# Optimization experiments

Measured on AMD Instinct MI355X. Metric: run time of the kernel, lower is better.

## Reference

```python
import jax, jax.numpy as jnp
import numpy as np
import math

B, L, HID = 2, 1024, 1536
NH, HD = 24, 64
DSSM = NH * HD            # 1536 (expand = 1)
QKV = 3 * DSSM
DCONV = 2
EPS = 1e-6


def _silu(u):
    return u * jax.nn.sigmoid(u)


def setup_inputs() -> dict:
    key = jax.random.key(0)
    ks = jax.random.split(key, 10)
    x = jax.random.normal(ks[0], (B, L, HID), dtype=jnp.float32)
    w_qkv = jax.random.normal(ks[1], (QKV, HID), dtype=jnp.float32) / math.sqrt(HID)
    conv_w = jax.random.normal(ks[2], (QKV, DCONV), dtype=jnp.float32) * 0.5  # depthwise causal conv, k=2
    w_dt = jax.random.normal(ks[3], (NH, HID), dtype=jnp.float32) * 0.02
    # dt_bias init exactly as in the torch module
    dt = jnp.exp(jax.random.uniform(ks[4], (NH,)) * (math.log(0.1) - math.log(0.001)) + math.log(0.001))
    dt = jnp.clip(dt, 1e-4, None)
    dt_bias = dt + jnp.log(-jnp.expm1(-dt))
    a_log = jnp.log(jax.random.uniform(ks[5], (NH,), minval=1.0, maxval=16.0))
    D = jnp.ones((NH, HD), dtype=jnp.float32)
    w_z = jax.random.normal(ks[6], (DSSM, HID), dtype=jnp.float32) / math.sqrt(HID)
    b_z = jnp.zeros((DSSM,), dtype=jnp.float32)
    rms_w = jnp.ones((DSSM,), dtype=jnp.float32)
    w_o = jax.random.normal(ks[7], (HID, DSSM), dtype=jnp.float32) / math.sqrt(DSSM)
    return dict(x=x, w_qkv=w_qkv, conv_w=conv_w, w_dt=w_dt, dt_bias=dt_bias,
                a_log=a_log, D=D, w_z=w_z, b_z=b_z, rms_w=rms_w, w_o=w_o)


def reference(x, w_qkv, conv_w, w_dt, dt_bias, a_log, D, w_z, b_z, rms_w, w_o):
    # qkv projection  [B,L,3*DSSM]
    qkv = jnp.einsum('blh,qh->blq', x, w_qkv)
    # depthwise causal conv1d (kernel size 2, padding k-1, trimmed to L)
    prev = jnp.pad(qkv, ((0, 0), (1, 0), (0, 0)))[:, :L]
    qkv = _silu(prev * conv_w[:, 0] + qkv * conv_w[:, 1])
    q, k, v = jnp.split(qkv, 3, axis=-1)
    q = q.reshape(B, L, NH, HD)
    k = k.reshape(B, L, NH, HD)
    v = v.reshape(B, L, NH, HD)
    # dt discretization: softplus(dt_proj(x) + dt_bias)   [B,L,NH]
    dt = jax.nn.softplus(jnp.einsum('blh,nh->bln', x, w_dt) + dt_bias)
    A = -jnp.exp(a_log)              # [NH], negative
    dA = dt * A                      # [B,L,NH]
    cs = jnp.transpose(jnp.cumsum(dA, axis=1), (0, 2, 1))   # [B,NH,L]
    diff = cs[:, :, :, None] - cs[:, :, None, :]            # [B,NH,L,L], <=0 on causal part
    causal = jnp.tril(jnp.ones((L, L), dtype=bool))
    decay = jnp.exp(jnp.where(causal, diff, -jnp.inf))      # segment-sum decay matrix
    # quadratic SSD (attention) form of the selective scan
    scores = jnp.einsum('bihd,bjhd->bhij', q, k) * decay
    scores = scores * jnp.transpose(dt, (0, 2, 1))[:, :, None, :]  # dt_j on keys (B-discretization)
    y = jnp.einsum('bhij,bjhd->bihd', scores, v)
    y = y + v * D                    # D skip connection
    y = y.reshape(B, L, DSSM)
    # z gate + RMSNorm + output projection
    z = jnp.einsum('blh,dh->bld', x, w_z) + b_z
    y = y * _silu(z)
    y = y * jax.lax.rsqrt(jnp.mean(y * y, axis=-1, keepdims=True) + EPS) * rms_w
    return jnp.einsum('bld,hd->blh', y, w_o)
```

## Files before the change

kernel.cpp:

```cpp
#include <hip/hip_runtime.h>
#include <hip/hip_bf16.h>
#include <math.h>

#define B_ 2
#define L_ 1024
#define HID_ 1536
#define NH_ 24
#define HD_ 64
#define DSSM_ 1536
#define QKV_ 4608
#define M_ 2048

typedef __attribute__((ext_vector_type(8))) short short8;
typedef __attribute__((ext_vector_type(4))) short short4e;
typedef __attribute__((ext_vector_type(4))) float floatx4;

__device__ __forceinline__ void gload_lds16(const short* g, short* l)
{
    __builtin_amdgcn_global_load_lds(
        (const __attribute__((address_space(1))) void*)g,
        (__attribute__((address_space(3))) void*)l,
        16, 0, 0);
}

__device__ __forceinline__ float bfs2f(short s)
{
    unsigned u = ((unsigned)(unsigned short)s) << 16;
    float f; __builtin_memcpy(&f, &u, 4); return f;
}
__device__ __forceinline__ short f2bfs(float f)
{
    __hip_bfloat16 h = __float2bfloat16(f);
    short s; __builtin_memcpy(&s, &h, 2); return s;
}

__device__ const int kIt[30] = {0,1,2,3,4,5, 6,6, 7,7, 8,8, 9,9, 10,10, 11,11,
                                12,12,12, 13,13,13, 14,14,14, 15,15,15};
__device__ const int kS[30]  = {0,0,0,0,0,0, 0,1, 0,1, 0,1, 0,1, 0,1, 0,1,
                                0,1,2, 0,1,2, 0,1,2, 0,1,2};

#define CN0 (M_ * HID_)
#define CN1 (QKV_ * HID_)
#define CN2 (DSSM_ * HID_)
#define CN3 (HID_ * DSSM_)
__global__ void cast_all_kernel(
    const float* __restrict__ x,  const float* __restrict__ wq,
    const float* __restrict__ wz, const float* __restrict__ wo,
    __hip_bfloat16* __restrict__ xb,
    __hip_bfloat16* __restrict__ wcat,
    __hip_bfloat16* __restrict__ wob)
{
    int i = (blockIdx.x * 256 + threadIdx.x) * 4;
    const float* src; __hip_bfloat16* dst; int off;
    if (i < CN0)                   { src = x;  dst = xb;         off = i; }
    else if (i < CN0 + CN1)        { src = wq; dst = wcat;       off = i - CN0; }
    else if (i < CN0 + CN1 + CN2)  { src = wz; dst = wcat + CN1; off = i - CN0 - CN1; }
    else                           { src = wo; dst = wob;        off = i - CN0 - CN1 - CN2; }
    float4 f = *reinterpret_cast<const float4*>(src + off);
    dst[off]     = __float2bfloat16(f.x);
    dst[off + 1] = __float2bfloat16(f.y);
    dst[off + 2] = __float2bfloat16(f.z);
    dst[off + 3] = __float2bfloat16(f.w);
}

#define MFMA_ __builtin_amdgcn_mfma_f32_16x16x32_bf16
#define BAR_() __builtin_amdgcn_s_barrier()
#define DRAIN_() do { asm volatile("s_waitcnt lgkmcnt(0)" ::: "memory"); \
                      __builtin_amdgcn_sched_barrier(0); } while (0)

#define CSTR 200

__global__ __launch_bounds__(512, 1) void gemm_qkvz_256(
    const __hip_bfloat16* __restrict__ A,
    const __hip_bfloat16* __restrict__ Bm,
    __hip_bfloat16* __restrict__ qkv_out,
    float* __restrict__ z_out,
    const float* __restrict__ b_z)
{
    extern __shared__ short lds[];
    const int K  = HID_;
    const int NT = K / 64;
    const int tid   = threadIdx.x;
    const int lane  = tid & 63;
    const int wave  = tid >> 6;
    const int col16 = lane & 15;
    const int quad  = lane >> 4;
    const int wm = wave >> 2;
    const int wn = wave & 3;
    const int rowblk = blockIdx.y * 256;
    const int colblk = blockIdx.x * 192;

    const short* Ap = reinterpret_cast<const short*>(A);
    const short* Bp = reinterpret_cast<const short*>(Bm);

    const int o  = tid * 16;
    const int s  = o ^ (((o >> 7) & 7) << 4);
    const int sr = s >> 7;
    const int sc = (s & 127) >> 1;
    const int ldst = tid * 8;

    const int mask = (col16 & 7) << 4;
    const int e0 = ((quad * 16)      ^ mask) >> 1;
    const int e1 = ((64 + quad * 16) ^ mask) >> 1;
    const int arow = (wm * 128 + col16) * 64;
    const int brow = (wn * 48  + col16) * 64;

    floatx4 acc[8][3] = {};

    auto STAGE_A = [&](int c, int u, int t) {
        const short* g = Ap + (size_t)(rowblk + u * 64 + sr) * K + t * 64 + sc;
        gload_lds16(g, &lds[c * 16384 + u * 4096 + ldst]);
    };
    auto STAGE_B = [&](int c, int u, int t) {
        const short* g = Bp + (size_t)(colblk + u * 64 + sr) * K + t * 64 + sc;
        gload_lds16(g, &lds[32768 + c * 12288 + u * 4096 + ldst]);
    };

    STAGE_A(0, 0, 0); STAGE_A(0, 1, 0); STAGE_A(0, 2, 0); STAGE_A(0, 3, 0);
    STAGE_B(0, 0, 0); STAGE_B(0, 1, 0); STAGE_B(0, 2, 0);
    STAGE_A(1, 0, 1); STAGE_A(1, 1, 1); STAGE_A(1, 2, 1); STAGE_A(1, 3, 1);
    asm volatile("s_waitcnt vmcnt(4)" ::: "memory");
    __builtin_amdgcn_sched_barrier(0);
    BAR_();

    for (int t = 0; t < NT; ++t) {
        const int cur = t & 1, nxt = cur ^ 1;
        const int Ab = cur * 16384;
        const int Bb = 32768 + cur * 12288;
        short8 af0[8], af1[8], bf0[3], bf1[3];

#pragma unroll
        for (int m = 0; m < 8; ++m)
            af0[m] = *reinterpret_cast<const short8*>(&lds[Ab + arow + m * 1024 + e0]);
#pragma unroll
        for (int n = 0; n < 3; ++n)
            bf0[n] = *reinterpret_cast<const short8*>(&lds[Bb + brow + n * 1024 + e0]);
        if (t + 1 < NT) { STAGE_B(nxt, 0, t + 1); STAGE_B(nxt, 1, t + 1); }
        BAR_();
        __builtin_amdgcn_s_setprio(1);
#pragma unroll
        for (int m = 0; m < 8; ++m) {
            acc[m][0] = MFMA_(af0[m], bf0[0], acc[m][0], 0, 0, 0);
            acc[m][1] = MFMA_(af0[m], bf0[1], acc[m][1], 0, 0, 0);
        }
        __builtin_amdgcn_s_setprio(0);
        DRAIN_();
        BAR_();

#pragma unroll
        for (int m = 0; m < 8; ++m)
            af1[m] = *reinterpret_cast<const short8*>(&lds[Ab + arow + m * 1024 + e1]);
        bf1[0] = *reinterpret_cast<const short8*>(&lds[Bb + brow + e1]);
        if (t + 1 < NT) STAGE_B(nxt, 2, t + 1);
        BAR_();
        __builtin_amdgcn_s_setprio(1);
#pragma unroll
        for (int m = 0; m < 8; ++m) {
            acc[m][2] = MFMA_(af0[m], bf0[2], acc[m][2], 0, 0, 0);
            acc[m][0] = MFMA_(af1[m], bf1[0], acc[m][0], 0, 0, 0);
        }
        __builtin_amdgcn_s_setprio(0);
        DRAIN_();
        BAR_();

        bf1[1] = *reinterpret_cast<const short8*>(&lds[Bb + brow + 1024 + e1]);
        bf1[2] = *reinterpret_cast<const short8*>(&lds[Bb + brow + 2048 + e1]);
        if (t + 2 < NT) {
            STAGE_A(cur, 0, t + 2); STAGE_A(cur, 1, t + 2);
            STAGE_A(cur, 2, t + 2); STAGE_A(cur, 3, t + 2);
        }
        if (t >= NT - 2) { asm volatile("s_waitcnt vmcnt(0)" ::: "memory"); }
        else             { asm volatile("s_waitcnt vmcnt(4)" ::: "memory"); }
        __builtin_amdgcn_sched_barrier(0);
        BAR_();
        __builtin_amdgcn_s_setprio(1);
#pragma unroll
        for (int m = 0; m < 8; ++m) {
            acc[m][1] = MFMA_(af1[m], bf1[1], acc[m][1], 0, 0, 0);
            acc[m][2] = MFMA_(af1[m], bf1[2], acc[m][2], 0, 0, 0);
        }
        __builtin_amdgcn_s_setprio(0);
        DRAIN_();
        BAR_();
    }

    if (blockIdx.x < 24) {
        const int rb = wm * 128 + quad * 4;
        const int cb = wn * 48 + col16;
#pragma unroll
        for (int m = 0; m < 8; ++m)
#pragma unroll
            for (int n = 0; n < 3; ++n)
#pragma unroll
                for (int r = 0; r < 4; ++r)
                    lds[(rb + m * 16 + r) * CSTR + cb + n * 16] =
                        f2bfs(acc[m][n][r]);
        __syncthreads();
        const int row = tid >> 1;
        const int seg = tid & 1;
        const short* srcp = &lds[row * CSTR + seg * 96];
        short* dstp = reinterpret_cast<short*>(qkv_out)
                    + (size_t)(rowblk + row) * QKV_ + colblk + seg * 96;
#pragma unroll
        for (int j = 0; j < 12; ++j)
            *reinterpret_cast<short8*>(dstp + j * 8) =
                *reinterpret_cast<const short8*>(srcp + j * 8);
    } else {
        const int row0  = rowblk + wm * 128;
        const int col0g = colblk + wn * 48 - QKV_;
#pragma unroll
        for (int m = 0; m < 8; ++m)
#pragma unroll
            for (int n = 0; n < 3; ++n)
#pragma unroll
                for (int r = 0; r < 4; ++r) {
                    int row = row0 + m * 16 + quad * 4 + r;
                    int col = col0g + n * 16 + col16;
                    z_out[(size_t)row * DSSM_ + col] = acc[m][n][r] + b_z[col];
                }
    }
}

template<int OUTMODE>
__global__ __launch_bounds__(256) void gemm_nt(
    const __hip_bfloat16* __restrict__ A,
    const __hip_bfloat16* __restrict__ Bm,
    void* __restrict__ Cv,
    const float* __restrict__ bias,
    int M, int N, int K)
{
    const int lane  = threadIdx.x & 63;
    const int wave  = threadIdx.x >> 6;
    const int col16 = lane & 15;
    const int quad  = lane >> 4;
    const int wr    = wave >> 1;
    const int wc    = wave & 1;
    const int rowblk = blockIdx.y * 128;
    const int colblk = blockIdx.x * 128;

    const short* Ap = reinterpret_cast<const short*>(A);
    const short* Bp = reinterpret_cast<const short*>(Bm);

    __shared__ alignas(16) short As[128 * 32];
    __shared__ alignas(16) short Bs[128 * 32];

    const int srow = lane >> 2;
    const int scol = (lane & 3) * 8;

    floatx4 acc[4][4] = {};

    for (int k0 = 0; k0 < K; k0 += 32) {
#pragma unroll
        for (int s2 = 0; s2 < 2; ++s2) {
            const int seg = wave * 2 + s2;
            gload_lds16(Ap + (size_t)(rowblk + seg * 16 + srow) * K + k0 + scol,
                        &As[seg * 512]);
            gload_lds16(Bp + (size_t)(colblk + seg * 16 + srow) * K + k0 + scol,
                        &Bs[seg * 512]);
        }
        __syncthreads();

        short8 af[4], bf[4];
#pragma unroll
        for (int t = 0; t < 4; ++t) {
            af[t] = *reinterpret_cast<const short8*>(
                &As[(wr * 64 + t * 16 + col16) * 32 + quad * 8]);
            bf[t] = *reinterpret_cast<const short8*>(
                &Bs[(wc * 64 + t * 16 + col16) * 32 + quad * 8]);
        }
#pragma unroll
        for (int mt = 0; mt < 4; ++mt)
#pragma unroll
            for (int nt = 0; nt < 4; ++nt)
                acc[mt][nt] = __builtin_amdgcn_mfma_f32_16x16x32_bf16(
                    af[mt], bf[nt], acc[mt][nt], 0, 0, 0);
        __syncthreads();
    }

    const int row0 = rowblk + wr * 64;
    const int col0 = colblk + wc * 64;
#pragma unroll
    for (int mt = 0; mt < 4; ++mt) {
#pragma unroll
        for (int nt = 0; nt < 4; ++nt) {
#pragma unroll
            for (int r = 0; r < 4; ++r) {
                int row = row0 + mt * 16 + quad * 4 + r;
                int col = col0 + nt * 16 + col16;
                float v = acc[mt][nt][r];
                if (OUTMODE == 1) v += bias[col];
                if (OUTMODE == 2)
                    ((__hip_bfloat16*)Cv)[(size_t)row * N + col] = __float2bfloat16(v);
                else
                    ((float*)Cv)[(size_t)row * N + col] = v;
            }
        }
    }
}

__global__ void conv_silu_kernel(
    const __hip_bfloat16* __restrict__ raw,
    const float* __restrict__ conv_w,
    __hip_bfloat16* __restrict__ q,
    __hip_bfloat16* __restrict__ k,
    __hip_bfloat16* __restrict__ v)
{
    int idx8 = blockIdx.x * 256 + threadIdx.x;
    int c8 = (idx8 % (QKV_ / 8)) * 8;
    int ml = idx8 / (QKV_ / 8);
    int l  = ml % L_;
    int b  = ml / L_;

    const short* base = reinterpret_cast<const short*>(raw) + (size_t)ml * QKV_ + c8;
    short8 curv = *reinterpret_cast<const short8*>(base);
    short8 prevv = {};
    if (l > 0) prevv = *reinterpret_cast<const short8*>(base - QKV_);

    float4 w0 = *reinterpret_cast<const float4*>(conv_w + c8 * 2);
    float4 w1 = *reinterpret_cast<const float4*>(conv_w + c8 * 2 + 4);
    float4 w2 = *reinterpret_cast<const float4*>(conv_w + c8 * 2 + 8);
    float4 w3 = *reinterpret_cast<const float4*>(conv_w + c8 * 2 + 12);
    const float wa[16] = {w0.x, w0.y, w0.z, w0.w, w1.x, w1.y, w1.z, w1.w,
                          w2.x, w2.y, w2.z, w2.w, w3.x, w3.y, w3.z, w3.w};

    short8 outv;
#pragma unroll
    for (int j = 0; j < 8; ++j) {
        float u = bfs2f(prevv[j]) * wa[2 * j] + bfs2f(curv[j]) * wa[2 * j + 1];
        u = fmaxf(u, -80.f);
        outv[j] = f2bfs(u / (1.f + __expf(-u)));
    }

    int part = c8 / DSSM_;
    int cc   = c8 % DSSM_;
    int nh   = cc >> 6;
    int d    = cc & 63;
    __hip_bfloat16* dst = (part == 0) ? q : ((part == 1) ? k : v);
    *reinterpret_cast<short8*>(
        reinterpret_cast<short*>(dst) + (((size_t)b * NH_ + nh) * L_ + l) * HD_ + d)
        = outv;
}

__global__ __launch_bounds__(256) void dtproj_kernel(
    const float* __restrict__ x,
    const float* __restrict__ w_dt,
    const float* __restrict__ dt_bias,
    const float* __restrict__ a_log,
    float* __restrict__ dt,
    float* __restrict__ dA)
{
    const int tid  = threadIdx.x;
    const int wave = tid >> 6;
    const int lane = tid & 63;
    const int m0   = blockIdx.x * 8 + wave * 2;

    float4 xa[2][6];
#pragma unroll
    for (int rr = 0; rr < 2; ++rr)
#pragma unroll
        for (int j = 0; j < 6; ++j)
            xa[rr][j] = *reinterpret_cast<const float4*>(
                x + (size_t)(m0 + rr) * HID_ + lane * 4 + j * 256);

    float acc0[NH_], acc1[NH_];
#pragma unroll
    for (int n = 0; n < NH_; ++n) {
        float s0 = 0.f, s1 = 0.f;
#pragma unroll
        for (int j = 0; j < 6; ++j) {
            float4 w = *reinterpret_cast<const float4*>(
                w_dt + (size_t)n * HID_ + lane * 4 + j * 256);
            s0 += xa[0][j].x * w.x + xa[0][j].y * w.y
                + xa[0][j].z * w.z + xa[0][j].w * w.w;
            s1 += xa[1][j].x * w.x + xa[1][j].y * w.y
                + xa[1][j].z * w.z + xa[1][j].w * w.w;
        }
        acc0[n] = s0;
        acc1[n] = s1;
    }

#pragma unroll
    for (int off = 32; off; off >>= 1) {
#pragma unroll
        for (int n = 0; n < NH_; ++n) {
            acc0[n] += __shfl_xor(acc0[n], off, 64);
            acc1[n] += __shfl_xor(acc1[n], off, 64);
        }
    }

    if (lane < NH_) {
        const int n = lane;
        float bias = dt_bias[n];
        float Aval = -__expf(a_log[n]);
        float v0 = acc0[n] + bias;
        float v1 = acc1[n] + bias;
        v0 = (v0 > 20.f) ? v0 : log1pf(__expf(v0));
        v1 = (v1 > 20.f) ? v1 : log1pf(__expf(v1));
        int b0 = m0 / L_, l0 = m0 % L_;
        size_t o0 = ((size_t)b0 * NH_ + n) * L_ + l0;
        dt[o0]     = v0;
        dA[o0]     = v0 * Aval;
        dt[o0 + 1] = v1;
        dA[o0 + 1] = v1 * Aval;
    }
}

__global__ void cumsum_kernel(const float* __restrict__ dA, float* __restrict__ cs)
{
    int bnh  = blockIdx.x;
    int lane = threadIdx.x;
    const float* src = dA + (size_t)bnh * L_;
    float* dst       = cs + (size_t)bnh * L_;

    float loc[16];
    float run = 0.f;
#pragma unroll
    for (int t = 0; t < 16; ++t) { run += src[lane * 16 + t]; loc[t] = run; }
    float tot = run;
    float sc = tot;
#pragma unroll
    for (int off = 1; off < 64; off <<= 1) {
        float o = __shfl_up(sc, off, 64);
        if (lane >= off) sc += o;
    }
    float offset = sc - tot;
#pragma unroll
    for (int t = 0; t < 16; ++t) dst[lane * 16 + t] = loc[t] + offset;
}

__global__ __launch_bounds__(256) void vdt_transpose_kernel(
    const __hip_bfloat16* __restrict__ v,
    const float* __restrict__ dt,
    __hip_bfloat16* __restrict__ vt)
{
    const int lt0 = blockIdx.x * 64;
    const int bnh = blockIdx.z * NH_ + blockIdx.y;
    const int tid = threadIdx.x;

    __shared__ short T[64][72];

    {
        int row = tid >> 2;
        int cc  = (tid & 3) * 16;
        const short* sp = reinterpret_cast<const short*>(v)
                        + ((size_t)bnh * L_ + lt0 + row) * HD_ + cc;
        float dtr = dt[(size_t)bnh * L_ + lt0 + row];
        short8 a = *reinterpret_cast<const short8*>(sp);
        short8 b = *reinterpret_cast<const short8*>(sp + 8);
#pragma unroll
        for (int j = 0; j < 8; ++j) {
            T[row][cc + j]     = f2bfs(bfs2f(a[j]) * dtr);
            T[row][cc + 8 + j] = f2bfs(bfs2f(b[j]) * dtr);
        }
    }
    __syncthreads();
    {
        int d  = tid >> 2;
        int lc = (tid & 3) * 16;
        short8 o0, o1;
#pragma unroll
        for (int j = 0; j < 8; ++j) {
            o0[j] = T[lc + j][d];
            o1[j] = T[lc + 8 + j][d];
        }
        short* dst = reinterpret_cast<short*>(vt)
                   + ((size_t)bnh * HD_ + d) * L_ + lt0 + lc;
        *reinterpret_cast<short8*>(dst)     = o0;
        *reinterpret_cast<short8*>(dst + 8) = o1;
    }
}

__global__ __launch_bounds__(256) void attn_kernel(
    const __hip_bfloat16* __restrict__ q,
    const __hip_bfloat16* __restrict__ k,
    const __hip_bfloat16* __restrict__ vt,
    const float* __restrict__ cs,
    float* __restrict__ p0,
    float* __restrict__ p1,
    float* __restrict__ p2)
{
    const int pidx = blockIdx.x;
    const int it   = kIt[pidx];
    const int sl   = kS[pidx];
    const int nh   = blockIdx.y;
    const int b    = blockIdx.z;
    const int tid  = threadIdx.x;
    const int lane = tid & 63;
    const int wave = tid >> 6;
    const int col  = lane & 15;
    const int quad = lane >> 4;
    const int bnh  = b * NH_ + nh;
    const int iw0  = it * 64 + wave * 16;

    float* pout = (sl == 0) ? p0 : ((sl == 1) ? p1 : p2);

    const short* qp  = reinterpret_cast<const short*>(q);
    const short* kp  = reinterpret_cast<const short*>(k);
    const short* vtp = reinterpret_cast<const short*>(vt);

    __shared__ alignas(16) short Ks[4096];
    __shared__ alignas(16) short Ps[4 * 16 * 72];

    const short* qrow = qp + ((size_t)bnh * L_ + iw0 + col) * HD_;
    short8 aq0 = *reinterpret_cast<const short8*>(qrow + quad * 8);
    short8 aq1 = *reinterpret_cast<const short8*>(qrow + 32 + quad * 8);

    float csr[4];
#pragma unroll
    for (int r = 0; r < 4; ++r)
        csr[r] = cs[(size_t)bnh * L_ + iw0 + quad * 4 + r];

    floatx4 accO[4] = {};

    const int jt_end = min(sl * 6 + 5, it);
    for (int jt = sl * 6; jt <= jt_end; ++jt) {
        const int j0 = jt * 64;
        {
            const short* gk = kp + ((size_t)bnh * L_ + j0 + wave * 16 + (lane >> 2)) * HD_
                            + (lane & 3) * 8;
            gload_lds16(gk,      &Ks[wave * 512 + lane * 8]);
            gload_lds16(gk + 32, &Ks[2048 + wave * 512 + lane * 8]);
        }
        __syncthreads();

#pragma unroll
        for (int s = 0; s < 4; ++s) {
            int jsub = j0 + s * 16;
            if (jsub <= iw0 + 15) {
                short8 bk0 = *reinterpret_cast<const short8*>(
                    &Ks[(s * 16 + col) * 32 + quad * 8]);
                short8 bk1 = *reinterpret_cast<const short8*>(
                    &Ks[2048 + (s * 16 + col) * 32 + quad * 8]);
                floatx4 sc = {};
                sc = __builtin_amdgcn_mfma_f32_16x16x32_bf16(aq0, bk0, sc, 0, 0, 0);
                sc = __builtin_amdgcn_mfma_f32_16x16x32_bf16(aq1, bk1, sc, 0, 0, 0);
                int j = jsub + col;
                float csj = cs[(size_t)bnh * L_ + j];
#pragma unroll
                for (int r = 0; r < 4; ++r) {
                    int i = iw0 + quad * 4 + r;
                    float e = (j <= i) ? __expf(csr[r] - csj) : 0.f;
                    Ps[wave * 1152 + (quad * 4 + r) * 72 + s * 16 + col] =
                        f2bfs(sc[r] * e);
                }
            } else if (j0 + (s >> 1) * 32 <= iw0 + 15) {
#pragma unroll
                for (int r = 0; r < 4; ++r)
                    Ps[wave * 1152 + (quad * 4 + r) * 72 + s * 16 + col] = 0;
            }
        }

#pragma unroll
        for (int c = 0; c < 2; ++c) {
            if (j0 + c * 32 > iw0 + 15) continue;
            short8 pa = *reinterpret_cast<const short8*>(
                &Ps[wave * 1152 + col * 72 + c * 32 + quad * 8]);
#pragma unroll
            for (int nt = 0; nt < 4; ++nt) {
                short8 bv = *reinterpret_cast<const short8*>(
                    vtp + ((size_t)bnh * HD_ + nt * 16 + col) * L_
                        + j0 + c * 32 + quad * 8);
                accO[nt] = __builtin_amdgcn_mfma_f32_16x16x32_bf16(pa, bv, accO[nt], 0, 0, 0);
            }
        }
        __syncthreads();
    }

#pragma unroll
    for (int nt = 0; nt < 4; ++nt) {
#pragma unroll
        for (int r = 0; r < 4; ++r) {
            int i  = iw0 + quad * 4 + r;
            int dv = nt * 16 + col;
            pout[((size_t)b * L_ + i) * DSSM_ + nh * HD_ + dv] = accO[nt][r];
        }
    }
}

__global__ __launch_bounds__(256) void gate_rms_kernel(
    const float* __restrict__ p0,
    const float* __restrict__ p1,
    const float* __restrict__ p2,
    const float* __restrict__ z,
    const __hip_bfloat16* __restrict__ v,
    const float* __restrict__ Dm,
    const float* __restrict__ rms_w,
    __hip_bfloat16* __restrict__ yn)
{
    int m   = blockIdx.x;
    int b   = m / L_;
    int l   = m % L_;
    int tid = threadIdx.x;
    size_t base = (size_t)m * DSSM_;
    const bool has1 = (l >= 384);
    const bool has2 = (l >= 768);

    floatx4 acc4[2] = {};
    float ss = 0.f;
#pragma unroll
    for (int t = 0; t < 2; ++t) {
        int i4 = t * 256 + tid;
        if (i4 < DSSM_ / 4) {
            int c  = i4 * 4;
            int nh = c >> 6, d = c & 63;
            floatx4 p = *reinterpret_cast<const floatx4*>(p0 + base + c);
            if (has1) p += *reinterpret_cast<const floatx4*>(p1 + base + c);
            if (has2) p += *reinterpret_cast<const floatx4*>(p2 + base + c);
            floatx4 dm = *reinterpret_cast<const floatx4*>(Dm + c);
            floatx4 zz = *reinterpret_cast<const floatx4*>(z + base + c);
            short4e vv = *reinterpret_cast<const short4e*>(
                reinterpret_cast<const short*>(v)
                + (((size_t)b * NH_ + nh) * L_ + l) * HD_ + d);
            floatx4 g;
#pragma unroll
            for (int j = 0; j < 4; ++j) {
                float yv = p[j] + bfs2f(vv[j]) * dm[j];
                float zv = fmaxf(zz[j], -80.f);
                float gv = yv * (zv / (1.f + __expf(-zv)));
                ss += gv * gv;
                g[j] = gv;
            }
            acc4[t] = g;
        }
    }
#pragma unroll
    for (int off = 32; off; off >>= 1) ss += __shfl_xor(ss, off, 64);
    __shared__ float red[4];
    if ((tid & 63) == 0) red[tid >> 6] = ss;
    __syncthreads();
    ss = red[0] + red[1] + red[2] + red[3];
    float r = rsqrtf(ss / (float)DSSM_ + 1e-6f);
#pragma unroll
    for (int t = 0; t < 2; ++t) {
        int i4 = t * 256 + tid;
        if (i4 < DSSM_ / 4) {
            int c = i4 * 4;
            floatx4 rw = *reinterpret_cast<const floatx4*>(rms_w + c);
            short4e o;
#pragma unroll
            for (int j = 0; j < 4; ++j)
                o[j] = f2bfs(acc4[t][j] * r * rw[j]);
            *reinterpret_cast<short4e*>(
                reinterpret_cast<short*>(yn) + base + c) = o;
        }
    }
}

extern "C" void kernel_launch(void* const* d_in, const int* in_sizes, int n_in,
                              void* d_out, int out_size, void* d_ws, size_t ws_size,
                              hipStream_t stream)
{
    const float* x       = (const float*)d_in[0];
    const float* w_qkv   = (const float*)d_in[1];
    const float* conv_w  = (const float*)d_in[2];
    const float* w_dt    = (const float*)d_in[3];
    const float* dt_bias = (const float*)d_in[4];
    const float* a_log   = (const float*)d_in[5];
    const float* Dm      = (const float*)d_in[6];
    const float* w_z     = (const float*)d_in[7];
    const float* b_z     = (const float*)d_in[8];
    const float* rms_w   = (const float*)d_in[9];
    const float* w_o     = (const float*)d_in[10];
    float* out = (float*)d_out;

    char* ws = (char*)d_ws;

    __hip_bfloat16* xb    = (__hip_bfloat16*)(ws);
    __hip_bfloat16* wob   = (__hip_bfloat16*)(ws + 6291456);
    float*          zbuf  = (float*)(ws + 11010048);
    __hip_bfloat16* wcat  = (__hip_bfloat16*)(ws + 23592960);
    __hip_bfloat16* qkvb  = (__hip_bfloat16*)(ws + 42467328);
    __hip_bfloat16* qb    = (__hip_bfloat16*)(ws + 61341696);
    __hip_bfloat16* kb    = (__hip_bfloat16*)(ws + 67633152);
    __hip_bfloat16* vb    = (__hip_bfloat16*)(ws + 73924608);
    float* dt   = (float*)(ws + 80216064);
    float* dA   = (float*)(ws + 80412672);
    float* cs   = (float*)(ws + 80609280);
    __hip_bfloat16* vtb = (__hip_bfloat16*)(ws);
    __hip_bfloat16* yn  = (__hip_bfloat16*)(ws);
    float* p0 = (float*)(ws + 23592960);
    float* p1 = (float*)(ws + 36175872);
    float* p2 = (float*)(ws + 48758784);

    static bool attr_set = false;
    if (!attr_set) {
        (void)hipFuncSetAttribute(reinterpret_cast<const void*>(gemm_qkvz_256),
                                  hipFuncAttributeMaxDynamicSharedMemorySize,
                                  114688);
        attr_set = true;
    }

    cast_all_kernel<<<(CN0 + CN1 + CN2 + CN3) / 1024, 256, 0, stream>>>(
        x, w_qkv, w_z, w_o, xb, wcat, wob);

    gemm_qkvz_256<<<dim3((QKV_ + DSSM_) / 192, M_ / 256), 512, 114688, stream>>>(
        xb, wcat, qkvb, zbuf, b_z);

    conv_silu_kernel<<<(B_ * L_ * QKV_ / 8) / 256, 256, 0, stream>>>(
        qkvb, conv_w, qb, kb, vb);

    dtproj_kernel<<<M_ / 8, 256, 0, stream>>>(x, w_dt, dt_bias, a_log, dt, dA);

    cumsum_kernel<<<B_ * NH_, 64, 0, stream>>>(dA, cs);

    vdt_transpose_kernel<<<dim3(L_ / 64, NH_, B_), 256, 0, stream>>>(vb, dt, vtb);

    attn_kernel<<<dim3(30, NH_, B_), 256, 0, stream>>>(
        qb, kb, vtb, cs, p0, p1, p2);

    gate_rms_kernel<<<M_, 256, 0, stream>>>(p0, p1, p2, zbuf, vb, Dm, rms_w, yn);

    gemm_nt<0><<<dim3(HID_ / 128, M_ / 128), 256, 0, stream>>>(
        yn, wob, (void*)out, nullptr, M_, HID_, DSSM_);
}
```

Measured before the change: 276.2 us.

## Remap waves to 4x2 grid and collapse GEMM k-loop into single phase

Changes the wave layout of the QKV/Z GEMM from 2x4 to 4x2, so each wave owns a 64x96 subtile (4x6 MFMA tiles) instead of 128x48. The three-phase k-iteration with interleaved LDS loads and staged global prefetch becomes one phase: load all A/B fragments, one barrier, issue every next-tile global->LDS load, then run all 48 MFMAs. This cuts the barriers per k-step from six to two and simplifies scheduling, but gives up the finer overlap of LDS reads with MFMAs and raises register pressure for fragments.

```diff
diff --git a/kernel.cpp b/kernel.cpp
--- a/kernel.cpp
+++ b/kernel.cpp
@@ -65,8 +65,6 @@
 
 #define MFMA_ __builtin_amdgcn_mfma_f32_16x16x32_bf16
 #define BAR_() __builtin_amdgcn_s_barrier()
-#define DRAIN_() do { asm volatile("s_waitcnt lgkmcnt(0)" ::: "memory"); \
-                      __builtin_amdgcn_sched_barrier(0); } while (0)
 
 #define CSTR 200
 
@@ -85,8 +83,8 @@
     const int wave  = tid >> 6;
     const int col16 = lane & 15;
     const int quad  = lane >> 4;
-    const int wm = wave >> 2;
-    const int wn = wave & 3;
+    const int wm = wave >> 1;
+    const int wn = wave & 1;
     const int rowblk = blockIdx.y * 256;
     const int colblk = blockIdx.x * 192;
 
@@ -102,10 +100,10 @@
     const int mask = (col16 & 7) << 4;
     const int e0 = ((quad * 16)      ^ mask) >> 1;
     const int e1 = ((64 + quad * 16) ^ mask) >> 1;
-    const int arow = (wm * 128 + col16) * 64;
-    const int brow = (wn * 48  + col16) * 64;
-
-    floatx4 acc[8][3] = {};
+    const int arow = (wm * 64 + col16) * 64;
+    const int brow = (wn * 96 + col16) * 64;
+
+    floatx4 acc[4][6] = {};
 
     auto STAGE_A = [&](int c, int u, int t) {
         const short* g = Ap + (size_t)(rowblk + u * 64 + sr) * K + t * 64 + sc;
@@ -127,70 +125,53 @@
         const int cur = t & 1, nxt = cur ^ 1;
         const int Ab = cur * 16384;
         const int Bb = 32768 + cur * 12288;
-        short8 af0[8], af1[8], bf0[3], bf1[3];
-
-#pragma unroll
-        for (int m = 0; m < 8; ++m)
+        short8 af0[4], af1[4], bf0[6], bf1[6];
+
+#pragma unroll
+        for (int m = 0; m < 4; ++m) {
             af0[m] = *reinterpret_cast<const short8*>(&lds[Ab + arow + m * 1024 + e0]);
-#pragma unroll
-        for (int n = 0; n < 3; ++n)
+            af1[m] = *reinterpret_cast<const short8*>(&lds[Ab + arow + m * 1024 + e1]);
+        }
+#pragma unroll
+        for (int n = 0; n < 6; ++n) {
             bf0[n] = *reinterpret_cast<const short8*>(&lds[Bb + brow + n * 1024 + e0]);
-        if (t + 1 < NT) { STAGE_B(nxt, 0, t + 1); STAGE_B(nxt, 1, t + 1); }
+            bf1[n] = *reinterpret_cast<const short8*>(&lds[Bb + brow + n * 1024 + e1]);
+        }
+        asm volatile("s_waitcnt lgkmcnt(0)" ::: "memory");
+        __builtin_amdgcn_sched_barrier(0);
         BAR_();
-        __builtin_amdgcn_s_setprio(1);
-#pragma unroll
-        for (int m = 0; m < 8; ++m) {
-            acc[m][0] = MFMA_(af0[m], bf0[0], acc[m][0], 0, 0, 0);
-            acc[m][1] = MFMA_(af0[m], bf0[1], acc[m][1], 0, 0, 0);
-        }
-        __builtin_amdgcn_s_setprio(0);
-        DRAIN_();
-        BAR_();
-
-#pragma unroll
-        for (int m = 0; m < 8; ++m)
-            af1[m] = *reinterpret_cast<const short8*>(&lds[Ab + arow + m * 1024 + e1]);
-        bf1[0] = *reinterpret_cast<const short8*>(&lds[Bb + brow + e1]);
-        if (t + 1 < NT) STAGE_B(nxt, 2, t + 1);
-        BAR_();
-        __builtin_amdgcn_s_setprio(1);
-#pragma unroll
-        for (int m = 0; m < 8; ++m) {
-            acc[m][2] = MFMA_(af0[m], bf0[2], acc[m][2], 0, 0, 0);
-            acc[m][0] = MFMA_(af1[m], bf1[0], acc[m][0], 0, 0, 0);
-        }
-        __builtin_amdgcn_s_setprio(0);
-        DRAIN_();
-        BAR_();
-
-        bf1[1] = *reinterpret_cast<const short8*>(&lds[Bb + brow + 1024 + e1]);
-        bf1[2] = *reinterpret_cast<const short8*>(&lds[Bb + brow + 2048 + e1]);
+
+        if (t + 1 < NT) {
+            STAGE_B(nxt, 0, t + 1); STAGE_B(nxt, 1, t + 1); STAGE_B(nxt, 2, t + 1);
+        }
         if (t + 2 < NT) {
             STAGE_A(cur, 0, t + 2); STAGE_A(cur, 1, t + 2);
             STAGE_A(cur, 2, t + 2); STAGE_A(cur, 3, t + 2);
         }
+
+        __builtin_amdgcn_s_setprio(1);
+#pragma unroll
+        for (int m = 0; m < 4; ++m)
+#pragma unroll
+            for (int n = 0; n < 6; ++n) {
+                acc[m][n] = MFMA_(af0[m], bf0[n], acc[m][n], 0, 0, 0);
+                acc[m][n] = MFMA_(af1[m], bf1[n], acc[m][n], 0, 0, 0);
+            }
+        __builtin_amdgcn_s_setprio(0);
+
         if (t >= NT - 2) { asm volatile("s_waitcnt vmcnt(0)" ::: "memory"); }
         else             { asm volatile("s_waitcnt vmcnt(4)" ::: "memory"); }
         __builtin_amdgcn_sched_barrier(0);
         BAR_();
-        __builtin_amdgcn_s_setprio(1);
-#pragma unroll
-        for (int m = 0; m < 8; ++m) {
-            acc[m][1] = MFMA_(af1[m], bf1[1], acc[m][1], 0, 0, 0);
-            acc[m][2] = MFMA_(af1[m], bf1[2], acc[m][2], 0, 0, 0);
-        }
-        __builtin_amdgcn_s_setprio(0);
-        DRAIN_();
-        BAR_();
     }
 
     if (blockIdx.x < 24) {
-        const int rb = wm * 128 + quad * 4;
-        const int cb = wn * 48 + col16;
-#pragma unroll
-        for (int m = 0; m < 8; ++m)
-#pragma unroll
-            for (int n = 0; n < 3; ++n)
+        const int rb = wm * 64 + quad * 4;
+        const int cb = wn * 96 + col16;
+#pragma unroll
+        for (int m = 0; m < 4; ++m)
+#pragma unroll
+            for (int n = 0; n < 6; ++n)
 #pragma unroll
                 for (int r = 0; r < 4; ++r)
                     lds[(rb + m * 16 + r) * CSTR + cb + n * 16] =
@@ -206,12 +187,12 @@
             *reinterpret_cast<short8*>(dstp + j * 8) =
                 *reinterpret_cast<const short8*>(srcp + j * 8);
     } else {
-        const int row0  = rowblk + wm * 128;
-        const int col0g = colblk + wn * 48 - QKV_;
-#pragma unroll
-        for (int m = 0; m < 8; ++m)
-#pragma unroll
-            for (int n = 0; n < 3; ++n)
+        const int row0  = rowblk + wm * 64;
+        const int col0g = colblk + wn * 96 - QKV_;
+#pragma unroll
+        for (int m = 0; m < 4; ++m)
+#pragma unroll
+            for (int n = 0; n < 6; ++n)
 #pragma unroll
                 for (int r = 0; r < 4; ++r) {
                     int row = row0 + m * 16 + quad * 4 + r;
```

Result: no change. 276.2 us (+0.0%).
